# Optimization experiments

Hardware: AMD Instinct MI355X
Metric: run time of the kernel (lower is better)

Reference implementation:

```python
import jax, jax.numpy as jnp
import numpy as np

EPS = 1e-12  # torch F.normalize default eps


def _l2norm(t, axis=-1):
    n = jnp.sqrt(jnp.sum(t * t, axis=axis, keepdims=True))
    return t / jnp.maximum(n, EPS)


def setup_inputs() -> dict:
    key = jax.random.key(0)
    ks = jax.random.split(key, 5)
    B, N, C, H = 8, 4096, 1024, 16
    x = jax.random.normal(ks[0], (B, N, C), dtype=jnp.float32)
    # nn.Linear(dim, 3*dim, bias=False): weight [3C, C]; we store transposed [C, 3C]
    w_qkv = jax.random.normal(ks[1], (C, 3 * C), dtype=jnp.float32) * (1.0 / np.sqrt(C))
    temperature = jnp.ones((H, 1, 1), dtype=jnp.float32)
    w_proj = jax.random.normal(ks[2], (C, C), dtype=jnp.float32) * (1.0 / np.sqrt(C))
    b_proj = jax.random.normal(ks[3], (C,), dtype=jnp.float32) * 0.01
    return {"x": x, "w_qkv": w_qkv, "temperature": temperature,
            "w_proj": w_proj, "b_proj": b_proj}


def reference(x, w_qkv, temperature, w_proj, b_proj):
    B, N, C = x.shape
    H = temperature.shape[0]
    dh = C // H
    # qkv: [B, N, 3C] -> [B, N, 3, H, dh] -> q/k/v each [B, H, dh, N]
    qkv = (x @ w_qkv).reshape(B, N, 3, H, dh).transpose(2, 0, 3, 4, 1)
    q, k, v = qkv[0], qkv[1], qkv[2]
    # L2-normalize over token axis (last dim)
    q = _l2norm(q)
    k = _l2norm(k)
    # channel-channel attention: [B, H, dh, dh]
    attn = jnp.einsum("bhdn,bhen->bhde", q, k) * temperature  # temp broadcasts [H,1,1]
    attn = jax.nn.softmax(attn, axis=-1)
    # weighted sum over channels: [B, H, dh, N] -> [B, N, C]
    out = jnp.einsum("bhde,bhen->bhdn", attn, v).transpose(0, 3, 1, 2).reshape(B, N, C)
    return out @ w_proj + b_proj
```

## Files before the change

### kernel.cpp

```cpp
#include <hip/hip_runtime.h>
#include <cstdint>

typedef unsigned short u16;
typedef unsigned int u32;
typedef __attribute__((ext_vector_type(8))) short bf16x8;
typedef __attribute__((ext_vector_type(4))) float f32x4;

typedef const u32 __attribute__((address_space(1)))* gp_t;
typedef u32 __attribute__((address_space(3)))* lp_t;

__device__ __forceinline__ u16 f2bf(float f) {
    union { float f; u32 u; } v; v.f = f;
    u32 r = v.u + 0x7FFFu + ((v.u >> 16) & 1u);
    return (u16)(r >> 16);
}
__device__ __forceinline__ float bf2f(u16 h) {
    union { u32 u; float f; } v; v.u = ((u32)h) << 16;
    return v.f;
}

__global__ __launch_bounds__(256) void k_pack2(const float* __restrict__ x,
                                               u16* __restrict__ xt, u16* __restrict__ xc) {
    __shared__ u16 tb[64][72];
    const int blk = blockIdx.x;
    const int tt = blk >> 4, ct = blk & 15;
    const long tok0 = (long)tt * 64;
    const int ch0 = ct * 64;
    const int tid = threadIdx.x;
    const int row = tid >> 2, cq = tid & 3;
#pragma unroll
    for (int jj = 0; jj < 4; ++jj) {
        const float4 v = *(const float4*)(x + (tok0 + row) * 1024 + ch0 + cq * 16 + jj * 4);
        tb[row][cq * 16 + jj * 4 + 0] = f2bf(v.x);
        tb[row][cq * 16 + jj * 4 + 1] = f2bf(v.y);
        tb[row][cq * 16 + jj * 4 + 2] = f2bf(v.z);
        tb[row][cq * 16 + jj * 4 + 3] = f2bf(v.w);
    }
    __syncthreads();
#pragma unroll
    for (int s = 0; s < 2; ++s) {
        const int c = s * 256 + tid;
        const int r2 = c >> 3, col8 = c & 7;
        *(uint4*)(xt + (tok0 + r2) * 1024 + ch0 + col8 * 8) = *(const uint4*)(&tb[r2][col8 * 8]);
    }
    const int b = (int)(tok0 >> 12);
    const int nin = (int)(tok0 & 4095);
#pragma unroll
    for (int s = 0; s < 2; ++s) {
        const int c = s * 256 + tid;
        const int crow = c >> 3, t8 = c & 7;
        u16 u[8];
#pragma unroll
        for (int k = 0; k < 8; ++k) u[k] = tb[t8 * 8 + k][crow];
        *(uint4*)(xc + ((long)b * 1024 + ch0 + crow) * 4096 + nin + t8 * 8) = *(const uint4*)u;
    }
}

__global__ void k_transpose_w(const float* __restrict__ src, u16* __restrict__ dst, int ncols) {
    __shared__ float t[64][65];
    int ntn = ncols >> 6;
    int kb = (blockIdx.x / ntn) * 64;
    int nb = (blockIdx.x % ntn) * 64;
    for (int i = threadIdx.x; i < 4096; i += 256) {
        int r = i >> 6, c = i & 63;
        t[r][c] = src[(long)(kb + r) * ncols + nb + c];
    }
    __syncthreads();
    for (int i = threadIdx.x; i < 4096; i += 256) {
        int r = i >> 6, c = i & 63;
        dst[(long)(nb + r) * 1024 + kb + c] = f2bf(t[c][r]);
    }
}

__global__ __launch_bounds__(256) void k_pack_wv(const float* __restrict__ wqkv, u16* __restrict__ wvb) {
    const int idx = blockIdx.x * 256 + threadIdx.x;
    const int cin = idx >> 7, e0 = (idx & 127) * 8;
    const float4 v1 = *(const float4*)(wqkv + (long)cin * 3072 + 2048 + e0);
    const float4 v2 = *(const float4*)(wqkv + (long)cin * 3072 + 2048 + e0 + 4);
    u16 u[8];
    u[0] = f2bf(v1.x); u[1] = f2bf(v1.y); u[2] = f2bf(v1.z); u[3] = f2bf(v1.w);
    u[4] = f2bf(v2.x); u[5] = f2bf(v2.y); u[6] = f2bf(v2.z); u[7] = f2bf(v2.w);
    *(uint4*)(wvb + (long)cin * 1024 + e0) = *(const uint4*)u;
}

template<int SYM>
__global__ __launch_bounds__(256) void k_g128(
    const u16* __restrict__ A, long Ab, const u16* __restrict__ Bt, long Bs,
    u16* __restrict__ C, long Cb, int K, int MT, int NT)
{
    __shared__ u16 sm[8192];
    __shared__ u16 lC[128 * 136];

    const int tid = threadIdx.x;
    const int wid = tid >> 6, lane = tid & 63;
    const int wr = wid >> 1, wc = wid & 1;
    const int fr = lane & 15, sl = lane >> 4;

    const int nwg = gridDim.x;
    const int logical = (blockIdx.x & 7) * (nwg >> 3) + (blockIdx.x >> 3);

    int b, i0, j0;
    if (SYM) {
        const int per = MT * (MT + 1) / 2;
        b = logical / per;
        int t = logical % per;
        int i = 0;
        while (t >= MT - i) { t -= MT - i; ++i; }
        i0 = i; j0 = i + t;
    } else {
        b = logical / (MT * NT);
        const int r = logical % (MT * NT);
        i0 = r / NT; j0 = r % NT;
    }
    const int m0 = i0 * 128, n0 = j0 * 128;
    const u16* Abp = A + (long)b * Ab;
    const u16* Bbp = Bt + (long)b * Bs;
    u16* Cbp = C + (long)b * Cb;

    const int srow = lane >> 2;
    const int sslot = lane & 3;

    f32x4 acc[4][4];
#pragma unroll
    for (int i = 0; i < 4; ++i)
#pragma unroll
        for (int j = 0; j < 4; ++j) acc[i][j] = (f32x4){0.f, 0.f, 0.f, 0.f};

    for (int kt = 0; kt < K; kt += 32) {
        __syncthreads();
#pragma unroll
        for (int i = 0; i < 2; ++i) {
            const int row = wid * 32 + i * 16 + srow;
            const int swz = (sslot ^ ((row >> 1) & 3)) << 3;
            const u16* ga = Abp + (long)(m0 + row) * K + kt + swz;
            const u16* gb = Bbp + (long)(n0 + row) * K + kt + swz;
            __builtin_amdgcn_global_load_lds((gp_t)ga, (lp_t)(sm + (wid * 2 + i) * 512), 16, 0, 0);
            __builtin_amdgcn_global_load_lds((gp_t)gb, (lp_t)(sm + 4096 + (wid * 2 + i) * 512), 16, 0, 0);
        }
        __syncthreads();
        bf16x8 af[4], bfr[4];
#pragma unroll
        for (int mi = 0; mi < 4; ++mi) {
            const int row = wr * 64 + mi * 16 + fr;
            af[mi] = *(const bf16x8*)(sm + row * 32 + ((sl ^ ((row >> 1) & 3)) << 3));
        }
#pragma unroll
        for (int ni = 0; ni < 4; ++ni) {
            const int row = wc * 64 + ni * 16 + fr;
            bfr[ni] = *(const bf16x8*)(sm + 4096 + row * 32 + ((sl ^ ((row >> 1) & 3)) << 3));
        }
#pragma unroll
        for (int mi = 0; mi < 4; ++mi)
#pragma unroll
            for (int ni = 0; ni < 4; ++ni)
                acc[mi][ni] = __builtin_amdgcn_mfma_f32_16x16x32_bf16(af[mi], bfr[ni], acc[mi][ni], 0, 0, 0);
    }
    __syncthreads();

#pragma unroll
    for (int mi = 0; mi < 4; ++mi)
#pragma unroll
        for (int ni = 0; ni < 4; ++ni) {
            const int ch = wc * 64 + ni * 16 + fr;
            const int tk = wr * 64 + mi * 16 + sl * 4;
#pragma unroll
            for (int rr = 0; rr < 4; ++rr)
                lC[(tk + rr) * 136 + ch] = f2bf(acc[mi][ni][rr]);
        }
    __syncthreads();
    {
        const int tk = tid >> 1, half = tid & 1;
        const u16* sp = lC + tk * 136 + half * 64;
        u16* dp = Cbp + (long)(m0 + tk) * 1024 + n0 + half * 64;
#pragma unroll
        for (int i = 0; i < 8; ++i) ((uint4*)dp)[i] = ((const uint4*)sp)[i];
    }
    if (SYM && i0 != j0) {
        __syncthreads();
#pragma unroll
        for (int mi = 0; mi < 4; ++mi)
#pragma unroll
            for (int ni = 0; ni < 4; ++ni) {
                const int ch = wc * 64 + ni * 16 + fr;
                const int tk = wr * 64 + mi * 16 + sl * 4;
                ushort4 w;
                w.x = f2bf(acc[mi][ni][0]); w.y = f2bf(acc[mi][ni][1]);
                w.z = f2bf(acc[mi][ni][2]); w.w = f2bf(acc[mi][ni][3]);
                *(ushort4*)(lC + ch * 136 + tk) = w;
            }
        __syncthreads();
        const int rw = tid >> 1, half = tid & 1;
        const u16* sp = lC + rw * 136 + half * 64;
        u16* dp = Cbp + (long)(n0 + rw) * 1024 + m0 + half * 64;
#pragma unroll
        for (int i = 0; i < 8; ++i) ((uint4*)dp)[i] = ((const uint4*)sp)[i];
    }
}

template<int EPI>
__global__ __launch_bounds__(512, 2) void k_gemm256(
    const u16* __restrict__ A, long Ab, const u16* __restrict__ Bt, long Bs,
    int MT, int NT,
    u16* __restrict__ cB, float* __restrict__ cF, long Cb, const float* __restrict__ bias)
{
    __shared__ uint4 smem4[8704];
    u16* sm = (u16*)smem4;

    const int tid = threadIdx.x;
    const int wid = tid >> 6, lane = tid & 63;
    const int wr = wid >> 2, wc = wid & 3;
    const int fr = lane & 15, sl = lane >> 4;

    const int nwg = gridDim.x;
    const int logical = (blockIdx.x & 7) * (nwg >> 3) + (blockIdx.x >> 3);
    const int b = logical / (MT * NT);
    const int rem = logical % (MT * NT);
    const int mt = rem / NT, nt = rem % NT;
    const long m0 = (long)mt * 256;
    const int n0 = nt * 256;

    const int srow = wid * 32 + (lane >> 2);
    const int kswz = (((lane & 3) ^ ((srow >> 1) & 3)) << 3);
    const u16* gA = A + (long)b * Ab + (m0 + srow) * 1024L + kswz;
    const u16* gB = Bt + (long)b * Bs + ((long)n0 + srow) * 1024L + kswz;
    const int ldst = wid * 1024;

    const int fxor = ((sl ^ ((fr >> 1) & 3)) << 3);
    const int aBase = (wr * 128 + fr) * 32 + fxor;
    const int bBase = 32768 + (wc * 64 + fr) * 32 + fxor;

    f32x4 acc[8][4];
#pragma unroll
    for (int i = 0; i < 8; ++i)
#pragma unroll
        for (int j = 0; j < 4; ++j) acc[i][j] = (f32x4){0.f, 0.f, 0.f, 0.f};

#define STAGE_A(d, kh, ts) do { \
    const u16* g_ = gA + (ts) * 64 + (kh) * 32; \
    u16* l_ = sm + (d) * 16384 + (kh) * 8192 + ldst; \
    __builtin_amdgcn_global_load_lds((gp_t)g_, (lp_t)l_, 16, 0, 0); \
    __builtin_amdgcn_global_load_lds((gp_t)(g_ + 16 * 1024), (lp_t)(l_ + 512), 16, 0, 0); \
} while (0)
#define STAGE_B(d, kh, ts) do { \
    const u16* g_ = gB + (ts) * 64 + (kh) * 32; \
    u16* l_ = sm + 32768 + (d) * 16384 + (kh) * 8192 + ldst; \
    __builtin_amdgcn_global_load_lds((gp_t)g_, (lp_t)l_, 16, 0, 0); \
    __builtin_amdgcn_global_load_lds((gp_t)(g_ + 16 * 1024), (lp_t)(l_ + 512), 16, 0, 0); \
} while (0)

    STAGE_A(0, 0, 0); STAGE_B(0, 0, 0);
    STAGE_A(0, 1, 0); STAGE_B(0, 1, 0);
    STAGE_A(1, 0, 1); STAGE_B(1, 0, 1);
    asm volatile("s_waitcnt vmcnt(8)" ::: "memory");
    __builtin_amdgcn_s_barrier();

    bf16x8 afX[4], afY[4], bfX[4], bfY[4];
#pragma unroll
    for (int ni = 0; ni < 4; ++ni) bfX[ni] = *(const bf16x8*)(sm + bBase + ni * 512);
#pragma unroll
    for (int mi = 0; mi < 4; ++mi) afX[mi] = *(const bf16x8*)(sm + aBase + mi * 512);

#pragma unroll 2
    for (int T = 0; T < 16; ++T) {
        const int d = T & 1;
        const int t1 = (T + 1 < 16) ? T + 1 : 15;
        const int t2 = (T + 2 < 16) ? T + 2 : 15;
        const int base = d * 16384;
        const int nbase = (d ^ 1) * 16384;

#pragma unroll
        for (int mi = 0; mi < 4; ++mi)
            afY[mi] = *(const bf16x8*)(sm + aBase + (4 + mi) * 512 + base);
        STAGE_A(d ^ 1, 1, t1);
        asm volatile("s_waitcnt vmcnt(6)" ::: "memory");
        __builtin_amdgcn_s_barrier();
        __builtin_amdgcn_s_setprio(1);
#pragma unroll
        for (int mi = 0; mi < 4; ++mi)
#pragma unroll
            for (int ni = 0; ni < 4; ++ni)
                acc[mi][ni] = __builtin_amdgcn_mfma_f32_16x16x32_bf16(afX[mi], bfX[ni], acc[mi][ni], 0, 0, 0);
        __builtin_amdgcn_s_setprio(0);
        __builtin_amdgcn_s_barrier();

#pragma unroll
        for (int ni = 0; ni < 4; ++ni)
            bfY[ni] = *(const bf16x8*)(sm + bBase + ni * 512 + base + 8192);
#pragma unroll
        for (int mi = 0; mi < 4; ++mi)
            afX[mi] = *(const bf16x8*)(sm + aBase + mi * 512 + base + 8192);
        STAGE_B(d ^ 1, 1, t1);
        __builtin_amdgcn_s_barrier();
        __builtin_amdgcn_s_setprio(1);
#pragma unroll
        for (int mi = 0; mi < 4; ++mi)
#pragma unroll
            for (int ni = 0; ni < 4; ++ni)
                acc[mi + 4][ni] = __builtin_amdgcn_mfma_f32_16x16x32_bf16(afY[mi], bfX[ni], acc[mi + 4][ni], 0, 0, 0);
        __builtin_amdgcn_s_setprio(0);
        __builtin_amdgcn_s_barrier();

#pragma unroll
        for (int mi = 0; mi < 4; ++mi)
            afY[mi] = *(const bf16x8*)(sm + aBase + (4 + mi) * 512 + base + 8192);
        STAGE_A(d, 0, t2);
        asm volatile("s_waitcnt vmcnt(6)" ::: "memory");
        __builtin_amdgcn_s_barrier();
        __builtin_amdgcn_s_setprio(1);
#pragma unroll
        for (int mi = 0; mi < 4; ++mi)
#pragma unroll
            for (int ni = 0; ni < 4; ++ni)
                acc[mi][ni] = __builtin_amdgcn_mfma_f32_16x16x32_bf16(afX[mi], bfY[ni], acc[mi][ni], 0, 0, 0);
        __builtin_amdgcn_s_setprio(0);
        __builtin_amdgcn_s_barrier();

#pragma unroll
        for (int ni = 0; ni < 4; ++ni)
            bfX[ni] = *(const bf16x8*)(sm + bBase + ni * 512 + nbase);
#pragma unroll
        for (int mi = 0; mi < 4; ++mi)
            afX[mi] = *(const bf16x8*)(sm + aBase + mi * 512 + nbase);
        STAGE_B(d, 0, t2);
        __builtin_amdgcn_s_barrier();
        __builtin_amdgcn_s_setprio(1);
#pragma unroll
        for (int mi = 0; mi < 4; ++mi)
#pragma unroll
            for (int ni = 0; ni < 4; ++ni)
                acc[mi + 4][ni] = __builtin_amdgcn_mfma_f32_16x16x32_bf16(afY[mi], bfY[ni], acc[mi + 4][ni], 0, 0, 0);
        __builtin_amdgcn_s_setprio(0);
        __builtin_amdgcn_s_barrier();
    }
#undef STAGE_A
#undef STAGE_B
    asm volatile("s_waitcnt vmcnt(0)" ::: "memory");
    __syncthreads();

    if (EPI == 0) {
        u16* cbase = cB + (long)b * Cb;
        u16* piece = sm + wid * 8704;
#pragma unroll
        for (int mi = 0; mi < 8; ++mi)
#pragma unroll
            for (int ni = 0; ni < 4; ++ni) {
                const int ch = ni * 16 + fr;
                const int tk = mi * 16 + sl * 4;
#pragma unroll
                for (int rr = 0; rr < 4; ++rr)
                    piece[(tk + rr) * 68 + ch] = f2bf(acc[mi][ni][rr]);
            }
        __syncthreads();
#pragma unroll
        for (int i = 0; i < 32; ++i) {
            const int chunk = i * 512 + tid;
            const int row = chunk >> 4, c8 = chunk & 15;
            const int p = row >> 7, tk = row & 127;
            const int wrp = p >> 2, wcp = p & 3;
            const uint2 v = *(const uint2*)(sm + p * 8704 + tk * 68 + c8 * 4);
            *(uint2*)(cbase + (m0 + wrp * 128 + tk) * 1024L + n0 + wcp * 64 + c8 * 4) = v;
        }
    } else {
        float* cbase = cF + (long)b * Cb;
        float bi[4];
#pragma unroll
        for (int ni = 0; ni < 4; ++ni) bi[ni] = bias[n0 + wc * 64 + ni * 16 + fr];
#pragma unroll
        for (int pass = 0; pass < 2; ++pass) {
            float* pieceF = (float*)smem4 + wid * 4352;
            if (pass) __syncthreads();
#pragma unroll
            for (int mi2 = 0; mi2 < 4; ++mi2) {
                const int mi = pass * 4 + mi2;
#pragma unroll
                for (int ni = 0; ni < 4; ++ni) {
                    const int ch = ni * 16 + fr;
                    const int tk = mi2 * 16 + sl * 4;
#pragma unroll
                    for (int rr = 0; rr < 4; ++rr)
                        pieceF[(tk + rr) * 68 + ch] = acc[mi][ni][rr] + bi[ni];
                }
            }
            __syncthreads();
#pragma unroll
            for (int i = 0; i < 16; ++i) {
                const int chunk = i * 512 + tid;
                const int row = chunk >> 4, c4 = chunk & 15;
                const int p = row >> 6, tk = row & 63;
                const int wrp = p >> 2, wcp = p & 3;
                const float4 v = *(const float4*)((float*)smem4 + p * 4352 + tk * 68 + c4 * 4);
                *(float4*)(cbase + (m0 + wrp * 128 + pass * 64 + tk) * 1024L + n0 + wcp * 64 + c4 * 4) = v;
            }
        }
    }
}

__global__ __launch_bounds__(256) void k_gram2(
    const u16* __restrict__ wqT, const u16* __restrict__ Ut,
    const float* __restrict__ temperature, u16* __restrict__ attn_g)
{
    __shared__ float lS[64 * 65];
    __shared__ float lsq[128];

    const int bh = blockIdx.x;
    const int b = bh >> 4, h = bh & 15;
    const int tid = threadIdx.x;
    const int wid = tid >> 6, lane = tid & 63;
    const int fr = lane & 15, sl = lane >> 4;

    {
        const int row = tid >> 1, half = tid & 1;
        const int j = (row < 64) ? (h * 64 + row) : (1024 + h * 64 + (row - 64));
        const u16* pa = wqT + (long)j * 1024 + half * 512;
        const u16* pb = Ut + ((long)b * 2048 + j) * 1024 + half * 512;
        float s = 0.f;
#pragma unroll 4
        for (int i = 0; i < 64; ++i) {
            const uint4 a = *(const uint4*)(pa + i * 8);
            const uint4 bv = *(const uint4*)(pb + i * 8);
            s += bf2f((u16)(a.x & 0xFFFF)) * bf2f((u16)(bv.x & 0xFFFF));
            s += bf2f((u16)(a.x >> 16))    * bf2f((u16)(bv.x >> 16));
            s += bf2f((u16)(a.y & 0xFFFF)) * bf2f((u16)(bv.y & 0xFFFF));
            s += bf2f((u16)(a.y >> 16))    * bf2f((u16)(bv.y >> 16));
            s += bf2f((u16)(a.z & 0xFFFF)) * bf2f((u16)(bv.z & 0xFFFF));
            s += bf2f((u16)(a.z >> 16))    * bf2f((u16)(bv.z >> 16));
            s += bf2f((u16)(a.w & 0xFFFF)) * bf2f((u16)(bv.w & 0xFFFF));
            s += bf2f((u16)(a.w >> 16))    * bf2f((u16)(bv.w >> 16));
        }
        s += __shfl_xor(s, 1);
        if (half == 0) lsq[row] = s;
    }

    const int d0 = wid * 16;
    f32x4 acc[4];
#pragma unroll
    for (int i = 0; i < 4; ++i) acc[i] = (f32x4){0.f, 0.f, 0.f, 0.f};

    const u16* aRow = wqT + (long)(h * 64 + d0 + fr) * 1024 + sl * 8;
    const u16* bRow = Ut + ((long)b * 2048 + 1024 + h * 64 + fr) * 1024 + sl * 8;
#pragma unroll 4
    for (int kb = 0; kb < 32; ++kb) {
        const bf16x8 a = *(const bf16x8*)(aRow + kb * 32);
#pragma unroll
        for (int ni = 0; ni < 4; ++ni) {
            const bf16x8 bb = *(const bf16x8*)(bRow + (long)ni * 16384 + kb * 32);
            acc[ni] = __builtin_amdgcn_mfma_f32_16x16x32_bf16(a, bb, acc[ni], 0, 0, 0);
        }
    }
#pragma unroll
    for (int ni = 0; ni < 4; ++ni)
#pragma unroll
        for (int rr = 0; rr < 4; ++rr)
            lS[(d0 + sl * 4 + rr) * 65 + ni * 16 + fr] = acc[ni][rr];
    __syncthreads();

    const float temp = temperature[h];
    const float rk = 1.f / fmaxf(sqrtf(lsq[64 + lane]), 1e-12f);
#pragma unroll 2
    for (int i = 0; i < 16; ++i) {
        const int d = wid * 16 + i;
        const float rq = 1.f / fmaxf(sqrtf(lsq[d]), 1e-12f);
        const float v = lS[d * 65 + lane] * rq * rk * temp;
        float mx = v;
#pragma unroll
        for (int o = 32; o; o >>= 1) mx = fmaxf(mx, __shfl_xor(mx, o));
        const float p = __expf(v - mx);
        float sum = p;
#pragma unroll
        for (int o = 32; o; o >>= 1) sum += __shfl_xor(sum, o);
        attn_g[(long)bh * 4096 + d * 64 + lane] = f2bf(p / sum);
    }
}

__global__ __launch_bounds__(256) void k_wmix(
    const u16* __restrict__ attn_g, const u16* __restrict__ wpT, u16* __restrict__ wmix)
{
    __shared__ u16 lA[64 * 72];
    __shared__ u16 lB[256 * 64];

    const int blk = blockIdx.x;
    const int nseg = blk & 3, bh = blk >> 2;
    const int b = bh >> 4, h = bh & 15;
    const int tid = threadIdx.x;
    const int wid = tid >> 6, lane = tid & 63;
    const int fr = lane & 15, sl = lane >> 4;

#pragma unroll
    for (int i = 0; i < 8; ++i) {
        const int cc = wid * 8 + i;
        const int row = cc * 8 + (lane >> 3);
        const int slot = lane & 7;
        const u16* g = wpT + (long)(nseg * 256 + row) * 1024 + h * 64 + ((slot ^ (row & 7)) << 3);
        __builtin_amdgcn_global_load_lds((gp_t)g, (lp_t)(lB + cc * 512), 16, 0, 0);
    }
    {
        const u16* src = attn_g + (long)bh * 4096;
        for (int i = tid; i < 4096; i += 256) {
            const int d = i >> 6, e = i & 63;
            lA[e * 72 + d] = src[i];
        }
    }
    __syncthreads();

    f32x4 acc[4][4];
#pragma unroll
    for (int i = 0; i < 4; ++i)
#pragma unroll
        for (int j = 0; j < 4; ++j) acc[i][j] = (f32x4){0.f, 0.f, 0.f, 0.f};

#pragma unroll
    for (int ks = 0; ks < 2; ++ks) {
        bf16x8 a[4], bb[4];
#pragma unroll
        for (int mi = 0; mi < 4; ++mi)
            a[mi] = *(const bf16x8*)(lA + (mi * 16 + fr) * 72 + ks * 32 + sl * 8);
#pragma unroll
        for (int ni = 0; ni < 4; ++ni) {
            const int rb = wid * 64 + ni * 16 + fr;
            bb[ni] = *(const bf16x8*)(lB + rb * 64 + (((ks * 4 + sl) ^ (rb & 7)) << 3));
        }
#pragma unroll
        for (int mi = 0; mi < 4; ++mi)
#pragma unroll
            for (int ni = 0; ni < 4; ++ni)
                acc[mi][ni] = __builtin_amdgcn_mfma_f32_16x16x32_bf16(a[mi], bb[ni], acc[mi][ni], 0, 0, 0);
    }

    u16* dst = wmix + ((long)b << 20);
#pragma unroll
    for (int mi = 0; mi < 4; ++mi)
#pragma unroll
        for (int ni = 0; ni < 4; ++ni) {
            const int cout = nseg * 256 + wid * 64 + ni * 16 + fr;
            const int e0 = mi * 16 + sl * 4;
            ushort4 w;
            w.x = f2bf(acc[mi][ni][0]); w.y = f2bf(acc[mi][ni][1]);
            w.z = f2bf(acc[mi][ni][2]); w.w = f2bf(acc[mi][ni][3]);
            *(ushort4*)(dst + (long)cout * 1024 + h * 64 + e0) = w;
        }
}

extern "C" void kernel_launch(void* const* d_in, const int* in_sizes, int n_in,
                              void* d_out, int out_size, void* d_ws, size_t ws_size,
                              hipStream_t stream) {
    const float* x = (const float*)d_in[0];
    const float* w_qkv = (const float*)d_in[1];
    const float* temperature = (const float*)d_in[2];
    const float* w_proj = (const float*)d_in[3];
    const float* b_proj = (const float*)d_in[4];
    float* out = (float*)d_out;
    char* ws = (char*)d_ws;

    u16* wqT    = (u16*)(ws);
    u16* wpT    = (u16*)(ws + 6291456);
    u16* wvb    = (u16*)(ws + 8388608);
    u16* xt     = (u16*)(ws + 10485760);
    u16* xc     = (u16*)(ws + 77594624);
    u16* S      = (u16*)(ws + 144703488);
    u16* Ut     = (u16*)(ws + 161480704);
    u16* attn_g = (u16*)(ws + 195035136);
    u16* wmix   = (u16*)(ws + 196083712);
    u16* wfinT  = (u16*)(ws + 212860928);

    k_pack2<<<8192, 256, 0, stream>>>(x, xt, xc);
    k_transpose_w<<<768, 256, 0, stream>>>(w_qkv, wqT, 3072);
    k_transpose_w<<<256, 256, 0, stream>>>(w_proj, wpT, 1024);
    k_pack_wv<<<512, 256, 0, stream>>>(w_qkv, wvb);
    k_g128<1><<<288, 256, 0, stream>>>(xc, 4194304L, xc, 4194304L, S, 1048576L, 4096, 8, 0);
    k_gemm256<0><<<256, 512, 0, stream>>>(wqT, 0L, S, 1048576L, 8, 4, Ut, nullptr, 2097152L, nullptr);
    k_gram2<<<128, 256, 0, stream>>>(wqT, Ut, temperature, attn_g);
    k_wmix<<<512, 256, 0, stream>>>(attn_g, wpT, wmix);
    k_g128<0><<<512, 256, 0, stream>>>(wmix, 1048576L, wvb, 0L, wfinT, 1048576L, 1024, 8, 8);
    k_gemm256<1><<<512, 512, 0, stream>>>(xt, 4194304L, wfinT, 1048576L, 16, 4, nullptr, out, 4194304L, b_proj);
}
```

Before: 384.7 us.

## Split-K the symmetric Gram GEMM and the per-head gram kernel across more workgroups

The symmetric X^T X GEMM (288 blocks, K=4096) is split into 4 K-segments (1152 blocks) that write fp32 partials, followed by a reduction kernel that sums them, converts to bf16 and writes both triangles. The per-head gram/softmax kernel (128 blocks) is likewise split into 4 K-segments staged through LDS, with a separate softmax kernel that reduces the partial gram and squared norms. The intent is to fill the GPU's CUs, which the old grids left underoccupied. The cost is extra fp32 partial-buffer traffic and two more kernel launches. The Sp partial buffer aliases Ut, which is only written after the reduction, so the reuse is safe.

```diff
diff --git a/kernel.cpp b/kernel.cpp
--- a/kernel.cpp
+++ b/kernel.cpp
@@ -83,7 +83,117 @@
     *(uint4*)(wvb + (long)cin * 1024 + e0) = *(const uint4*)u;
 }
 
-template<int SYM>
+__global__ __launch_bounds__(256) void k_g128p(
+    const u16* __restrict__ xc, float* __restrict__ Sp)
+{
+    __shared__ u16 sm[8192];
+
+    const int tid = threadIdx.x;
+    const int wid = tid >> 6, lane = tid & 63;
+    const int wr = wid >> 1, wc = wid & 1;
+    const int fr = lane & 15, sl = lane >> 4;
+
+    const int nwg = gridDim.x;
+    const int logical = (blockIdx.x & 7) * (nwg >> 3) + (blockIdx.x >> 3);
+    const int kseg = logical & 3;
+    const int bt = logical >> 2;
+    const int b = bt / 36;
+    int t = bt % 36;
+    int i0 = 0;
+    while (t >= 8 - i0) { t -= 8 - i0; ++i0; }
+    const int j0 = i0 + t;
+    const int m0 = i0 * 128, n0 = j0 * 128;
+
+    const u16* base = xc + (long)b * 4194304 + kseg * 1024;
+
+    const int srow = lane >> 2;
+    const int sslot = lane & 3;
+
+    f32x4 acc[4][4];
+#pragma unroll
+    for (int i = 0; i < 4; ++i)
+#pragma unroll
+        for (int j = 0; j < 4; ++j) acc[i][j] = (f32x4){0.f, 0.f, 0.f, 0.f};
+
+    for (int kt = 0; kt < 1024; kt += 32) {
+        __syncthreads();
+#pragma unroll
+        for (int i = 0; i < 2; ++i) {
+            const int row = wid * 32 + i * 16 + srow;
+            const int swz = (sslot ^ ((row >> 1) & 3)) << 3;
+            const u16* ga = base + (long)(m0 + row) * 4096 + kt + swz;
+            const u16* gb = base + (long)(n0 + row) * 4096 + kt + swz;
+            __builtin_amdgcn_global_load_lds((gp_t)ga, (lp_t)(sm + (wid * 2 + i) * 512), 16, 0, 0);
+            __builtin_amdgcn_global_load_lds((gp_t)gb, (lp_t)(sm + 4096 + (wid * 2 + i) * 512), 16, 0, 0);
+        }
+        __syncthreads();
+        bf16x8 af[4], bfr[4];
+#pragma unroll
+        for (int mi = 0; mi < 4; ++mi) {
+            const int row = wr * 64 + mi * 16 + fr;
+            af[mi] = *(const bf16x8*)(sm + row * 32 + ((sl ^ ((row >> 1) & 3)) << 3));
+        }
+#pragma unroll
+        for (int ni = 0; ni < 4; ++ni) {
+            const int row = wc * 64 + ni * 16 + fr;
+            bfr[ni] = *(const bf16x8*)(sm + 4096 + row * 32 + ((sl ^ ((row >> 1) & 3)) << 3));
+        }
+#pragma unroll
+        for (int mi = 0; mi < 4; ++mi)
+#pragma unroll
+            for (int ni = 0; ni < 4; ++ni)
+                acc[mi][ni] = __builtin_amdgcn_mfma_f32_16x16x32_bf16(af[mi], bfr[ni], acc[mi][ni], 0, 0, 0);
+    }
+
+    float* gp = Sp + (long)logical * 16384;
+#pragma unroll
+    for (int mi = 0; mi < 4; ++mi)
+#pragma unroll
+        for (int ni = 0; ni < 4; ++ni)
+#pragma unroll
+            for (int rr = 0; rr < 4; ++rr)
+                gp[(wr * 64 + mi * 16 + sl * 4 + rr) * 128 + wc * 64 + ni * 16 + fr] = acc[mi][ni][rr];
+}
+
+__global__ __launch_bounds__(256) void k_sred(const float* __restrict__ Sp, u16* __restrict__ S)
+{
+    __shared__ u16 lC[128 * 136];
+    __shared__ u16 lCT[128 * 136];
+
+    const int tid = threadIdx.x;
+    const int nwg = gridDim.x;
+    const int logical = (blockIdx.x & 7) * (nwg >> 3) + (blockIdx.x >> 3);
+    const int b = logical / 36;
+    int t = logical % 36;
+    int i0 = 0;
+    while (t >= 8 - i0) { t -= 8 - i0; ++i0; }
+    const int j0 = i0 + t;
+    const int m0 = i0 * 128, n0 = j0 * 128;
+
+    const float* p = Sp + (long)logical * 65536;
+    for (int i = tid; i < 16384; i += 256) {
+        const float s = p[i] + p[i + 16384] + p[i + 32768] + p[i + 49152];
+        const u16 v = f2bf(s);
+        const int r_ = i >> 7, c_ = i & 127;
+        lC[r_ * 136 + c_] = v;
+        lCT[c_ * 136 + r_] = v;
+    }
+    __syncthreads();
+    const int tk = tid >> 1, half = tid & 1;
+    {
+        u16* dp = S + (long)b * 1048576 + (long)(m0 + tk) * 1024 + n0 + half * 64;
+        const u16* sp1 = lC + tk * 136 + half * 64;
+#pragma unroll
+        for (int i = 0; i < 8; ++i) ((uint4*)dp)[i] = ((const uint4*)sp1)[i];
+    }
+    if (i0 != j0) {
+        u16* dp = S + (long)b * 1048576 + (long)(n0 + tk) * 1024 + m0 + half * 64;
+        const u16* sp2 = lCT + tk * 136 + half * 64;
+#pragma unroll
+        for (int i = 0; i < 8; ++i) ((uint4*)dp)[i] = ((const uint4*)sp2)[i];
+    }
+}
+
 __global__ __launch_bounds__(256) void k_g128(
     const u16* __restrict__ A, long Ab, const u16* __restrict__ Bt, long Bs,
     u16* __restrict__ C, long Cb, int K, int MT, int NT)
@@ -99,19 +209,9 @@
     const int nwg = gridDim.x;
     const int logical = (blockIdx.x & 7) * (nwg >> 3) + (blockIdx.x >> 3);
 
-    int b, i0, j0;
-    if (SYM) {
-        const int per = MT * (MT + 1) / 2;
-        b = logical / per;
-        int t = logical % per;
-        int i = 0;
-        while (t >= MT - i) { t -= MT - i; ++i; }
-        i0 = i; j0 = i + t;
-    } else {
-        b = logical / (MT * NT);
-        const int r = logical % (MT * NT);
-        i0 = r / NT; j0 = r % NT;
-    }
+    const int b = logical / (MT * NT);
+    const int r = logical % (MT * NT);
+    const int i0 = r / NT, j0 = r % NT;
     const int m0 = i0 * 128, n0 = j0 * 128;
     const u16* Abp = A + (long)b * Ab;
     const u16* Bbp = Bt + (long)b * Bs;
@@ -172,26 +272,6 @@
         const int tk = tid >> 1, half = tid & 1;
         const u16* sp = lC + tk * 136 + half * 64;
         u16* dp = Cbp + (long)(m0 + tk) * 1024 + n0 + half * 64;
-#pragma unroll
-        for (int i = 0; i < 8; ++i) ((uint4*)dp)[i] = ((const uint4*)sp)[i];
-    }
-    if (SYM && i0 != j0) {
-        __syncthreads();
-#pragma unroll
-        for (int mi = 0; mi < 4; ++mi)
-#pragma unroll
-            for (int ni = 0; ni < 4; ++ni) {
-                const int ch = wc * 64 + ni * 16 + fr;
-                const int tk = wr * 64 + mi * 16 + sl * 4;
-                ushort4 w;
-                w.x = f2bf(acc[mi][ni][0]); w.y = f2bf(acc[mi][ni][1]);
-                w.z = f2bf(acc[mi][ni][2]); w.w = f2bf(acc[mi][ni][3]);
-                *(ushort4*)(lC + ch * 136 + tk) = w;
-            }
-        __syncthreads();
-        const int rw = tid >> 1, half = tid & 1;
-        const u16* sp = lC + rw * 136 + half * 64;
-        u16* dp = Cbp + (long)(n0 + rw) * 1024 + m0 + half * 64;
 #pragma unroll
         for (int i = 0; i < 8; ++i) ((uint4*)dp)[i] = ((const uint4*)sp)[i];
     }
@@ -395,27 +475,42 @@
     }
 }
 
-__global__ __launch_bounds__(256) void k_gram2(
+__global__ __launch_bounds__(256) void k_gram2p(
     const u16* __restrict__ wqT, const u16* __restrict__ Ut,
-    const float* __restrict__ temperature, u16* __restrict__ attn_g)
+    float* __restrict__ g2p, float* __restrict__ sq2p)
 {
-    __shared__ float lS[64 * 65];
-    __shared__ float lsq[128];
-
-    const int bh = blockIdx.x;
+    __shared__ u16 lQ[64 * 256];
+    __shared__ u16 lK[64 * 256];
+
+    const int blk = blockIdx.x;
+    const int seg = blk & 3, bh = blk >> 2;
     const int b = bh >> 4, h = bh & 15;
     const int tid = threadIdx.x;
     const int wid = tid >> 6, lane = tid & 63;
-    const int fr = lane & 15, sl = lane >> 4;
+
+    {
+        const int r2 = lane >> 5, slot = lane & 31;
+        const int rbase = wid * 16;
+#pragma unroll
+        for (int i = 0; i < 8; ++i) {
+            const int r = rbase + i * 2 + r2;
+            const int col = seg * 256 + ((slot ^ (r & 7)) << 3);
+            const u16* gq = wqT + (long)(h * 64 + r) * 1024 + col;
+            const u16* gk = Ut + ((long)b * 2048 + 1024 + h * 64 + r) * 1024 + col;
+            __builtin_amdgcn_global_load_lds((gp_t)gq, (lp_t)(lQ + (rbase + i * 2) * 256), 16, 0, 0);
+            __builtin_amdgcn_global_load_lds((gp_t)gk, (lp_t)(lK + (rbase + i * 2) * 256), 16, 0, 0);
+        }
+    }
+    __syncthreads();
 
     {
         const int row = tid >> 1, half = tid & 1;
         const int j = (row < 64) ? (h * 64 + row) : (1024 + h * 64 + (row - 64));
-        const u16* pa = wqT + (long)j * 1024 + half * 512;
-        const u16* pb = Ut + ((long)b * 2048 + j) * 1024 + half * 512;
+        const u16* pa = wqT + (long)j * 1024 + seg * 256 + half * 128;
+        const u16* pb = Ut + ((long)b * 2048 + j) * 1024 + seg * 256 + half * 128;
         float s = 0.f;
 #pragma unroll 4
-        for (int i = 0; i < 64; ++i) {
+        for (int i = 0; i < 16; ++i) {
             const uint4 a = *(const uint4*)(pa + i * 8);
             const uint4 bv = *(const uint4*)(pb + i * 8);
             s += bf2f((u16)(a.x & 0xFFFF)) * bf2f((u16)(bv.x & 0xFFFF));
@@ -428,48 +523,60 @@
             s += bf2f((u16)(a.w >> 16))    * bf2f((u16)(bv.w >> 16));
         }
         s += __shfl_xor(s, 1);
-        if (half == 0) lsq[row] = s;
-    }
-
-    const int d0 = wid * 16;
+        if (half == 0) sq2p[(long)blk * 128 + row] = s;
+    }
+
+    const int fr = lane & 15, sl = lane >> 4;
     f32x4 acc[4];
 #pragma unroll
     for (int i = 0; i < 4; ++i) acc[i] = (f32x4){0.f, 0.f, 0.f, 0.f};
-
-    const u16* aRow = wqT + (long)(h * 64 + d0 + fr) * 1024 + sl * 8;
-    const u16* bRow = Ut + ((long)b * 2048 + 1024 + h * 64 + fr) * 1024 + sl * 8;
-#pragma unroll 4
-    for (int kb = 0; kb < 32; ++kb) {
-        const bf16x8 a = *(const bf16x8*)(aRow + kb * 32);
+#pragma unroll
+    for (int ks = 0; ks < 8; ++ks) {
+        const int ra = wid * 16 + fr;
+        const bf16x8 a = *(const bf16x8*)(lQ + ra * 256 + (((ks * 4 + sl) ^ (ra & 7)) << 3));
 #pragma unroll
         for (int ni = 0; ni < 4; ++ni) {
-            const bf16x8 bb = *(const bf16x8*)(bRow + (long)ni * 16384 + kb * 32);
+            const int rb = ni * 16 + fr;
+            const bf16x8 bb = *(const bf16x8*)(lK + rb * 256 + (((ks * 4 + sl) ^ (rb & 7)) << 3));
             acc[ni] = __builtin_amdgcn_mfma_f32_16x16x32_bf16(a, bb, acc[ni], 0, 0, 0);
         }
     }
+    float* gp = g2p + (long)blk * 4096;
 #pragma unroll
     for (int ni = 0; ni < 4; ++ni)
 #pragma unroll
         for (int rr = 0; rr < 4; ++rr)
-            lS[(d0 + sl * 4 + rr) * 65 + ni * 16 + fr] = acc[ni][rr];
-    __syncthreads();
-
-    const float temp = temperature[h];
-    const float rk = 1.f / fmaxf(sqrtf(lsq[64 + lane]), 1e-12f);
-#pragma unroll 2
-    for (int i = 0; i < 16; ++i) {
-        const int d = wid * 16 + i;
-        const float rq = 1.f / fmaxf(sqrtf(lsq[d]), 1e-12f);
-        const float v = lS[d * 65 + lane] * rq * rk * temp;
-        float mx = v;
-#pragma unroll
-        for (int o = 32; o; o >>= 1) mx = fmaxf(mx, __shfl_xor(mx, o));
-        const float p = __expf(v - mx);
-        float sum = p;
-#pragma unroll
-        for (int o = 32; o; o >>= 1) sum += __shfl_xor(sum, o);
-        attn_g[(long)bh * 4096 + d * 64 + lane] = f2bf(p / sum);
-    }
+            gp[(wid * 16 + sl * 4 + rr) * 64 + ni * 16 + fr] = acc[ni][rr];
+}
+
+__global__ __launch_bounds__(256) void k_smax2(
+    const float* __restrict__ g2p, const float* __restrict__ sq2p,
+    const float* __restrict__ temperature, u16* __restrict__ attn_g)
+{
+    const int row = blockIdx.x * 4 + (threadIdx.x >> 6);
+    const int e = threadIdx.x & 63;
+    const int bh = row >> 6, d = row & 63;
+    const int h = bh & 15;
+    float raw = 0.f, sqq = 0.f, sqk = 0.f;
+    const float* gp = g2p + (long)bh * 16384 + d * 64 + e;
+    const float* sp = sq2p + (long)bh * 512;
+#pragma unroll
+    for (int s = 0; s < 4; ++s) {
+        raw += gp[s * 4096];
+        sqq += sp[s * 128 + d];
+        sqk += sp[s * 128 + 64 + e];
+    }
+    const float rq = 1.f / fmaxf(sqrtf(sqq), 1e-12f);
+    const float rk = 1.f / fmaxf(sqrtf(sqk), 1e-12f);
+    const float v = raw * rq * rk * temperature[h];
+    float mx = v;
+#pragma unroll
+    for (int o = 32; o; o >>= 1) mx = fmaxf(mx, __shfl_xor(mx, o));
+    const float p = __expf(v - mx);
+    float sum = p;
+#pragma unroll
+    for (int o = 32; o; o >>= 1) sum += __shfl_xor(sum, o);
+    attn_g[(long)row * 64 + e] = f2bf(p / sum);
 }
 
 __global__ __launch_bounds__(256) void k_wmix(
@@ -557,19 +664,24 @@
     u16* xt     = (u16*)(ws + 10485760);
     u16* xc     = (u16*)(ws + 77594624);
     u16* S      = (u16*)(ws + 144703488);
+    float* Sp   = (float*)(ws + 161480704);
     u16* Ut     = (u16*)(ws + 161480704);
-    u16* attn_g = (u16*)(ws + 195035136);
-    u16* wmix   = (u16*)(ws + 196083712);
-    u16* wfinT  = (u16*)(ws + 212860928);
+    float* g2p  = (float*)(ws + 195035136);
+    float* sq2p = (float*)(ws + 203423744);
+    u16* attn_g = (u16*)(ws + 203685888);
+    u16* wmix   = (u16*)(ws + 204734464);
+    u16* wfinT  = (u16*)(ws + 221511680);
 
     k_pack2<<<8192, 256, 0, stream>>>(x, xt, xc);
     k_transpose_w<<<768, 256, 0, stream>>>(w_qkv, wqT, 3072);
     k_transpose_w<<<256, 256, 0, stream>>>(w_proj, wpT, 1024);
     k_pack_wv<<<512, 256, 0, stream>>>(w_qkv, wvb);
-    k_g128<1><<<288, 256, 0, stream>>>(xc, 4194304L, xc, 4194304L, S, 1048576L, 4096, 8, 0);
+    k_g128p<<<1152, 256, 0, stream>>>(xc, Sp);
+    k_sred<<<288, 256, 0, stream>>>(Sp, S);
     k_gemm256<0><<<256, 512, 0, stream>>>(wqT, 0L, S, 1048576L, 8, 4, Ut, nullptr, 2097152L, nullptr);
-    k_gram2<<<128, 256, 0, stream>>>(wqT, Ut, temperature, attn_g);
+    k_gram2p<<<512, 256, 0, stream>>>(wqT, Ut, g2p, sq2p);
+    k_smax2<<<2048, 256, 0, stream>>>(g2p, sq2p, temperature, attn_g);
     k_wmix<<<512, 256, 0, stream>>>(attn_g, wpT, wmix);
-    k_g128<0><<<512, 256, 0, stream>>>(wmix, 1048576L, wvb, 0L, wfinT, 1048576L, 1024, 8, 8);
+    k_g128<<<512, 256, 0, stream>>>(wmix, 1048576L, wvb, 0L, wfinT, 1048576L, 1024, 8, 8);
     k_gemm256<1><<<512, 512, 0, stream>>>(xt, 4194304L, wfinT, 1048576L, 16, 4, nullptr, out, 4194304L, b_proj);
 }
```

Result: faster. 345.6 us (-10.2%).
